# Optimization experiments

Measured on AMD Instinct MI355X. Metric: run time of the kernel, lower is better.

Reference implementation:

```python
import jax, jax.numpy as jnp
import numpy as np

N_NODES = 50000
N_EDGES = 150000
EMB = 64
IN_DIM = 32
LN_EPS = 1e-5


def setup_inputs() -> dict:
    key = jax.random.key(0)
    k1, k2, k3, k4 = jax.random.split(key, 4)
    h = jax.random.normal(k1, (N_NODES, EMB), dtype=jnp.float32)
    edge_attr = jax.random.normal(k2, (N_EDGES, IN_DIM), dtype=jnp.float32)
    edge_index = jax.random.randint(k3, (2, N_EDGES), 0, N_NODES, dtype=jnp.int64)
    # xavier_uniform for [EMB*EMB, IN_DIM] weight
    limit = float(np.sqrt(6.0 / (EMB * EMB + IN_DIM)))
    W = jax.random.uniform(k4, (EMB * EMB, IN_DIM), dtype=jnp.float32,
                           minval=-limit, maxval=limit)
    b = jnp.zeros((EMB * EMB,), dtype=jnp.float32)
    gamma = jnp.ones((EMB,), dtype=jnp.float32)
    beta = jnp.zeros((EMB,), dtype=jnp.float32)
    return {"h": h, "edge_attr": edge_attr, "W": W, "b": b,
            "gamma": gamma, "beta": beta, "edge_index": edge_index}


def reference(h, edge_attr, W, b, gamma, beta, edge_index):
    M = edge_attr.shape[0]
    E = h.shape[1]
    # per-edge transform matrix from edge features: [M, E, E]
    m = (edge_attr @ W.T + b).reshape(M, E, E)
    # gather target-node features and apply per-edge matvec: [M, E]
    h_j = h[edge_index[1]]
    msg = jnp.einsum('mef,mf->me', m, h_j)
    # scatter-add messages to source nodes
    aggr = jax.ops.segment_sum(msg, edge_index[0], num_segments=h.shape[0])
    # residual + LayerNorm
    x = h + aggr
    mu = jnp.mean(x, axis=-1, keepdims=True)
    var = jnp.mean(jnp.square(x - mu), axis=-1, keepdims=True)
    y = (x - mu) * jax.lax.rsqrt(var + LN_EPS)
    return y * gamma + beta
```

## Files before the change

kernel.cpp:

```cpp
#include <hip/hip_runtime.h>
#include <math.h>

#define N_NODES 50000
#define N_EDGES 150000
#define LN_EPS 1e-5f

#define BM 256
#define WM 64

typedef _Float16 f16x8 __attribute__((ext_vector_type(8)));
typedef _Float16 f16x4 __attribute__((ext_vector_type(4)));
typedef _Float16 f16x2 __attribute__((ext_vector_type(2)));
typedef float    f32x4 __attribute__((ext_vector_type(4)));

static __device__ __forceinline__ f16x2 pkrtz(float a, float b) {
    auto p = __builtin_amdgcn_cvt_pkrtz(a, b);
    f16x2 r; r[0] = (_Float16)p[0]; r[1] = (_Float16)p[1];
    return r;
}

__global__ void setup_kernel(const float* __restrict__ W, const float* __restrict__ b,
                             const float* __restrict__ h,
                             f16x8* __restrict__ WtF, float* __restrict__ out) {
    int bid = blockIdx.x;
    if (bid < 66) {
        int tid = bid * 256 + threadIdx.x;
        int l  = tid & 63;
        int nb = (tid >> 6) & 3;
        int c  = tid >> 8;
        int k0 = (l >> 4) << 3;
        int e  = nb * 16 + (l & 15);
        const float* src = (c < 64) ? &W[(e * 64 + c) * 32 + k0]
                                    : &b[e * 64 + (c - 64) * 32 + k0];
        float4 v0 = *(const float4*)src;
        float4 v1 = *(const float4*)(src + 4);
        f16x8 o;
        o[0] = (_Float16)v0.x; o[1] = (_Float16)v0.y; o[2] = (_Float16)v0.z; o[3] = (_Float16)v0.w;
        o[4] = (_Float16)v1.x; o[5] = (_Float16)v1.y; o[6] = (_Float16)v1.z; o[7] = (_Float16)v1.w;
        WtF[tid] = o;
    } else {
        int tid = (bid - 66) * 256 + threadIdx.x;
        ((float4*)out)[tid] = ((const float4*)h)[tid];
    }
}

__launch_bounds__(512, 4)
__global__ void edge_kernel(const float* __restrict__ ea,
                            const float* __restrict__ h,
                            const int*   __restrict__ ei,
                            const f16x8* __restrict__ WtF,
                            float* __restrict__ out)
{
    __shared__ _Float16 s_hj[BM][68];
    __shared__ int      s_src[BM];

    const int t = threadIdx.x;
    const int m_base = blockIdx.x * BM;

    {
        int row  = t >> 1;
        int half = t & 1;
        int gm   = m_base + row;
        if (gm < N_EDGES) {
            if (half == 0) s_src[row] = ei[gm];
            const float4* hr = (const float4*)&h[(size_t)ei[N_EDGES + gm] * 64 + half * 32];
            #pragma unroll
            for (int j = 0; j < 8; ++j) {
                float4 v = hr[j];
                f16x2 p0 = pkrtz(v.x, v.y);
                f16x2 p1 = pkrtz(v.z, v.w);
                f16x4 o; o[0] = p0[0]; o[1] = p0[1]; o[2] = p1[0]; o[3] = p1[1];
                *(f16x4*)&s_hj[row][half * 32 + j * 4] = o;
            }
        } else {
            if (half == 0) s_src[row] = -1;
            f16x4 z = (f16x4){0, 0, 0, 0};
            #pragma unroll
            for (int j = 0; j < 8; ++j)
                *(f16x4*)&s_hj[row][half * 32 + j * 4] = z;
        }
    }

    const int lane = t & 63;
    const int wid  = t >> 6;
    const int wrow = wid & 3;
    const int wn   = wid >> 2;
    const int nb0  = wn * 2;
    const int r16  = lane & 15;
    const int g    = lane >> 4;
    const int k0   = g * 8;
    const int row0 = wrow * WM;
    int rows[4];
    #pragma unroll
    for (int a = 0; a < 4; ++a) rows[a] = row0 + a * 16 + r16;

    f16x2 eap[4][4];
    #pragma unroll
    for (int a = 0; a < 4; ++a) {
        int gm = m_base + rows[a];
        if (gm < N_EDGES) {
            float4 v0 = *(const float4*)&ea[(size_t)gm * 32 + k0];
            float4 v1 = *(const float4*)&ea[(size_t)gm * 32 + k0 + 4];
            eap[a][0] = pkrtz(v0.x, v0.y);
            eap[a][1] = pkrtz(v0.z, v0.w);
            eap[a][2] = pkrtz(v1.x, v1.y);
            eap[a][3] = pkrtz(v1.z, v1.w);
        } else {
            #pragma unroll
            for (int i = 0; i < 4; ++i) eap[a][i] = (f16x2){0, 0};
        }
    }

    f32x4 acc[4][2];
    #pragma unroll
    for (int a = 0; a < 4; ++a)
        #pragma unroll
        for (int nb = 0; nb < 2; ++nb)
            acc[a][nb] = (f32x4){0.f, 0.f, 0.f, 0.f};

    __syncthreads();

    f16x8 b0[2], b1[2], b2[2];
    #pragma unroll
    for (int j = 0; j < 2; ++j) b0[j] = WtF[(0 * 4 + nb0 + j) * 64 + lane];
    #pragma unroll
    for (int j = 0; j < 2; ++j) b1[j] = WtF[(1 * 4 + nb0 + j) * 64 + lane];
    #pragma unroll
    for (int j = 0; j < 2; ++j) b2[j] = WtF[(2 * 4 + nb0 + j) * 64 + lane];

    _Float16 hc[4];
    #pragma unroll
    for (int a = 0; a < 4; ++a) hc[a] = s_hj[rows[a]][0];

    auto step = [&](int c, f16x8* bb, bool loadnext) {
        _Float16 hn[4] = {0, 0, 0, 0};
        if (loadnext) {
            #pragma unroll
            for (int a = 0; a < 4; ++a) hn[a] = s_hj[rows[a]][c + 1];
        }
        #pragma unroll
        for (int a = 0; a < 4; ++a) {
            f16x2 hs; hs[0] = hc[a]; hs[1] = hc[a];
            f16x2 p0 = eap[a][0] * hs;
            f16x2 p1 = eap[a][1] * hs;
            f16x2 p2 = eap[a][2] * hs;
            f16x2 p3 = eap[a][3] * hs;
            f16x8 va;
            va[0] = p0[0]; va[1] = p0[1]; va[2] = p1[0]; va[3] = p1[1];
            va[4] = p2[0]; va[5] = p2[1]; va[6] = p3[0]; va[7] = p3[1];
            #pragma unroll
            for (int j = 0; j < 2; ++j)
                acc[a][j] = __builtin_amdgcn_mfma_f32_16x16x32_f16(va, bb[j], acc[a][j], 0, 0, 0);
        }
        #pragma unroll
        for (int a = 0; a < 4; ++a) hc[a] = hn[a];
    };

    for (int c = 0; c < 63; c += 3) {
        step(c, b0, true);
        #pragma unroll
        for (int j = 0; j < 2; ++j) b0[j] = WtF[((c + 3) * 4 + nb0 + j) * 64 + lane];
        step(c + 1, b1, true);
        #pragma unroll
        for (int j = 0; j < 2; ++j) b1[j] = WtF[((c + 4) * 4 + nb0 + j) * 64 + lane];
        step(c + 2, b2, true);
        #pragma unroll
        for (int j = 0; j < 2; ++j) b2[j] = WtF[((c + 5) * 4 + nb0 + j) * 64 + lane];
    }
    step(63, b0, false);

    #pragma unroll
    for (int half = 0; half < 2; ++half) {
        f16x8* bb = half ? b2 : b1;
        #pragma unroll
        for (int a = 0; a < 4; ++a) {
            f16x4 lo = *(const f16x4*)&s_hj[rows[a]][half * 32 + k0];
            f16x4 hi = *(const f16x4*)&s_hj[rows[a]][half * 32 + k0 + 4];
            f16x8 va;
            va[0] = lo[0]; va[1] = lo[1]; va[2] = lo[2]; va[3] = lo[3];
            va[4] = hi[0]; va[5] = hi[1]; va[6] = hi[2]; va[7] = hi[3];
            #pragma unroll
            for (int j = 0; j < 2; ++j)
                acc[a][j] = __builtin_amdgcn_mfma_f32_16x16x32_f16(va, bb[j], acc[a][j], 0, 0, 0);
        }
    }

    #pragma unroll
    for (int a = 0; a < 4; ++a) {
        #pragma unroll
        for (int r = 0; r < 4; ++r) {
            int srcn = s_src[row0 + a * 16 + g * 4 + r];
            if (srcn >= 0) {
                #pragma unroll
                for (int j = 0; j < 2; ++j)
                    atomicAdd(&out[(size_t)srcn * 64 + (nb0 + j) * 16 + r16], acc[a][j][r]);
            }
        }
    }
}

__global__ void ln_kernel(const float* __restrict__ gamma, const float* __restrict__ beta,
                          float* __restrict__ out) {
    int row = blockIdx.x * 4 + (threadIdx.x >> 6);
    int lane = threadIdx.x & 63;
    if (row >= N_NODES) return;
    float x = out[row * 64 + lane];
    float s = x;
    #pragma unroll
    for (int o = 32; o; o >>= 1) s += __shfl_xor(s, o);
    float mu = s * (1.0f / 64.0f);
    float d = x - mu;
    float v = d * d;
    #pragma unroll
    for (int o = 32; o; o >>= 1) v += __shfl_xor(v, o);
    float var = v * (1.0f / 64.0f);
    float r = rsqrtf(var + LN_EPS);
    out[row * 64 + lane] = d * r * gamma[lane] + beta[lane];
}

extern "C" void kernel_launch(void* const* d_in, const int* in_sizes, int n_in,
                              void* d_out, int out_size, void* d_ws, size_t ws_size,
                              hipStream_t stream) {
    const float* h     = (const float*)d_in[0];
    const float* ea    = (const float*)d_in[1];
    const float* W     = (const float*)d_in[2];
    const float* b     = (const float*)d_in[3];
    const float* gamma = (const float*)d_in[4];
    const float* beta  = (const float*)d_in[5];
    const int*   ei    = (const int*)d_in[6];
    float* out = (float*)d_out;

    f16x8* WtF = (f16x8*)d_ws;

    setup_kernel<<<66 + 3125, 256, 0, stream>>>(W, b, h, WtF, out);
    edge_kernel<<<(N_EDGES + BM - 1) / BM, 512, 0, stream>>>(ea, h, ei, WtF, out);
    ln_kernel<<<(N_NODES + 3) / 4, 256, 0, stream>>>(gamma, beta, out);
}
```

Before: 163.0 us.

## Stage weights in LDS with double buffering, re-split warps, vectorize LayerNorm

The edge kernel now gives each warp 32 rows across all 64 output columns. It cooperatively stages the fp16 weight tiles into shared memory with double buffering and a block barrier per group of four columns, where before each warp read its own weight fragments straight from global memory. The bias tile is staged once into LDS. LayerNorm now uses 16 lanes per row with float4 accesses, and the copy of h processes two float4 per thread with bounds checks. This cuts redundant global/L2 weight traffic but adds LDS usage (about 68KB per block) and 16 barriers, which may lower occupancy.

Result: faster. 157.7 us (-3.2%).

```diff
diff --git a/kernel.cpp b/kernel.cpp
--- a/kernel.cpp
+++ b/kernel.cpp
@@ -6,7 +6,6 @@
 #define LN_EPS 1e-5f
 
 #define BM 256
-#define WM 64
 
 typedef _Float16 f16x8 __attribute__((ext_vector_type(8)));
 typedef _Float16 f16x4 __attribute__((ext_vector_type(4)));
@@ -39,8 +38,10 @@
         o[4] = (_Float16)v1.x; o[5] = (_Float16)v1.y; o[6] = (_Float16)v1.z; o[7] = (_Float16)v1.w;
         WtF[tid] = o;
     } else {
-        int tid = (bid - 66) * 256 + threadIdx.x;
-        ((float4*)out)[tid] = ((const float4*)h)[tid];
+        int base = (bid - 66) * 512 + threadIdx.x;
+        if (base < 800000) ((float4*)out)[base] = ((const float4*)h)[base];
+        int base2 = base + 256;
+        if (base2 < 800000) ((float4*)out)[base2] = ((const float4*)h)[base2];
     }
 }
 
@@ -53,6 +54,8 @@
 {
     __shared__ _Float16 s_hj[BM][68];
     __shared__ int      s_src[BM];
+    __shared__ f16x8    s_b[2][1024];
+    __shared__ f16x8    s_bias[512];
 
     const int t = threadIdx.x;
     const int m_base = blockIdx.x * BM;
@@ -83,20 +86,17 @@
 
     const int lane = t & 63;
     const int wid  = t >> 6;
-    const int wrow = wid & 3;
-    const int wn   = wid >> 2;
-    const int nb0  = wn * 2;
     const int r16  = lane & 15;
     const int g    = lane >> 4;
     const int k0   = g * 8;
-    const int row0 = wrow * WM;
-    int rows[4];
-    #pragma unroll
-    for (int a = 0; a < 4; ++a) rows[a] = row0 + a * 16 + r16;
-
-    f16x2 eap[4][4];
-    #pragma unroll
-    for (int a = 0; a < 4; ++a) {
+    const int row0 = wid * 32;
+    int rows[2];
+    rows[0] = row0 + r16;
+    rows[1] = row0 + 16 + r16;
+
+    f16x2 eap[2][4];
+    #pragma unroll
+    for (int a = 0; a < 2; ++a) {
         int gm = m_base + rows[a];
         if (gm < N_EDGES) {
             float4 v0 = *(const float4*)&ea[(size_t)gm * 32 + k0];
@@ -111,89 +111,90 @@
         }
     }
 
-    f32x4 acc[4][2];
-    #pragma unroll
-    for (int a = 0; a < 4; ++a)
-        #pragma unroll
-        for (int nb = 0; nb < 2; ++nb)
+    f32x4 acc[2][4];
+    #pragma unroll
+    for (int a = 0; a < 2; ++a)
+        #pragma unroll
+        for (int nb = 0; nb < 4; ++nb)
             acc[a][nb] = (f32x4){0.f, 0.f, 0.f, 0.f};
 
+    {
+        f16x8 rb = WtF[16384 + t];
+        f16x8 r0 = WtF[t];
+        f16x8 r1 = WtF[512 + t];
+        s_bias[t]        = rb;
+        s_b[0][t]        = r0;
+        s_b[0][512 + t]  = r1;
+    }
+
     __syncthreads();
 
-    f16x8 b0[2], b1[2], b2[2];
-    #pragma unroll
-    for (int j = 0; j < 2; ++j) b0[j] = WtF[(0 * 4 + nb0 + j) * 64 + lane];
-    #pragma unroll
-    for (int j = 0; j < 2; ++j) b1[j] = WtF[(1 * 4 + nb0 + j) * 64 + lane];
-    #pragma unroll
-    for (int j = 0; j < 2; ++j) b2[j] = WtF[(2 * 4 + nb0 + j) * 64 + lane];
-
-    _Float16 hc[4];
-    #pragma unroll
-    for (int a = 0; a < 4; ++a) hc[a] = s_hj[rows[a]][0];
-
-    auto step = [&](int c, f16x8* bb, bool loadnext) {
-        _Float16 hn[4] = {0, 0, 0, 0};
-        if (loadnext) {
-            #pragma unroll
-            for (int a = 0; a < 4; ++a) hn[a] = s_hj[rows[a]][c + 1];
-        }
-        #pragma unroll
-        for (int a = 0; a < 4; ++a) {
-            f16x2 hs; hs[0] = hc[a]; hs[1] = hc[a];
-            f16x2 p0 = eap[a][0] * hs;
-            f16x2 p1 = eap[a][1] * hs;
-            f16x2 p2 = eap[a][2] * hs;
-            f16x2 p3 = eap[a][3] * hs;
-            f16x8 va;
-            va[0] = p0[0]; va[1] = p0[1]; va[2] = p1[0]; va[3] = p1[1];
-            va[4] = p2[0]; va[5] = p2[1]; va[6] = p3[0]; va[7] = p3[1];
-            #pragma unroll
-            for (int j = 0; j < 2; ++j)
-                acc[a][j] = __builtin_amdgcn_mfma_f32_16x16x32_f16(va, bb[j], acc[a][j], 0, 0, 0);
-        }
-        #pragma unroll
-        for (int a = 0; a < 4; ++a) hc[a] = hn[a];
-    };
-
-    for (int c = 0; c < 63; c += 3) {
-        step(c, b0, true);
-        #pragma unroll
-        for (int j = 0; j < 2; ++j) b0[j] = WtF[((c + 3) * 4 + nb0 + j) * 64 + lane];
-        step(c + 1, b1, true);
-        #pragma unroll
-        for (int j = 0; j < 2; ++j) b1[j] = WtF[((c + 4) * 4 + nb0 + j) * 64 + lane];
-        step(c + 2, b2, true);
-        #pragma unroll
-        for (int j = 0; j < 2; ++j) b2[j] = WtF[((c + 5) * 4 + nb0 + j) * 64 + lane];
-    }
-    step(63, b0, false);
+    int buf = 0;
+    for (int grp = 0; grp < 16; ++grp) {
+        f16x8 ra, rb2;
+        if (grp < 15) {
+            ra  = WtF[(grp + 1) * 1024 + t];
+            rb2 = WtF[(grp + 1) * 1024 + 512 + t];
+        }
+        f16x4 hv[2];
+        hv[0] = *(const f16x4*)&s_hj[rows[0]][grp * 4];
+        hv[1] = *(const f16x4*)&s_hj[rows[1]][grp * 4];
+
+        #pragma unroll
+        for (int cc = 0; cc < 4; ++cc) {
+            f16x8 bf[4];
+            #pragma unroll
+            for (int nb = 0; nb < 4; ++nb)
+                bf[nb] = s_b[buf][(cc * 4 + nb) * 64 + lane];
+            #pragma unroll
+            for (int a = 0; a < 2; ++a) {
+                f16x2 hs; hs[0] = hv[a][cc]; hs[1] = hv[a][cc];
+                f16x2 p0 = eap[a][0] * hs;
+                f16x2 p1 = eap[a][1] * hs;
+                f16x2 p2 = eap[a][2] * hs;
+                f16x2 p3 = eap[a][3] * hs;
+                f16x8 va;
+                va[0] = p0[0]; va[1] = p0[1]; va[2] = p1[0]; va[3] = p1[1];
+                va[4] = p2[0]; va[5] = p2[1]; va[6] = p3[0]; va[7] = p3[1];
+                #pragma unroll
+                for (int nb = 0; nb < 4; ++nb)
+                    acc[a][nb] = __builtin_amdgcn_mfma_f32_16x16x32_f16(va, bf[nb], acc[a][nb], 0, 0, 0);
+            }
+        }
+        if (grp < 15) {
+            s_b[buf ^ 1][t]       = ra;
+            s_b[buf ^ 1][512 + t] = rb2;
+        }
+        __syncthreads();
+        buf ^= 1;
+    }
 
     #pragma unroll
     for (int half = 0; half < 2; ++half) {
-        f16x8* bb = half ? b2 : b1;
-        #pragma unroll
-        for (int a = 0; a < 4; ++a) {
+        #pragma unroll
+        for (int a = 0; a < 2; ++a) {
             f16x4 lo = *(const f16x4*)&s_hj[rows[a]][half * 32 + k0];
             f16x4 hi = *(const f16x4*)&s_hj[rows[a]][half * 32 + k0 + 4];
             f16x8 va;
             va[0] = lo[0]; va[1] = lo[1]; va[2] = lo[2]; va[3] = lo[3];
             va[4] = hi[0]; va[5] = hi[1]; va[6] = hi[2]; va[7] = hi[3];
             #pragma unroll
-            for (int j = 0; j < 2; ++j)
-                acc[a][j] = __builtin_amdgcn_mfma_f32_16x16x32_f16(va, bb[j], acc[a][j], 0, 0, 0);
-        }
-    }
-
-    #pragma unroll
-    for (int a = 0; a < 4; ++a) {
+            for (int nb = 0; nb < 4; ++nb) {
+                f16x8 bf = s_bias[(half * 4 + nb) * 64 + lane];
+                acc[a][nb] = __builtin_amdgcn_mfma_f32_16x16x32_f16(va, bf, acc[a][nb], 0, 0, 0);
+            }
+        }
+    }
+
+    #pragma unroll
+    for (int a = 0; a < 2; ++a) {
         #pragma unroll
         for (int r = 0; r < 4; ++r) {
             int srcn = s_src[row0 + a * 16 + g * 4 + r];
             if (srcn >= 0) {
                 #pragma unroll
-                for (int j = 0; j < 2; ++j)
-                    atomicAdd(&out[(size_t)srcn * 64 + (nb0 + j) * 16 + r16], acc[a][j][r]);
+                for (int nb = 0; nb < 4; ++nb)
+                    atomicAdd(&out[(size_t)srcn * 64 + nb * 16 + r16], acc[a][nb][r]);
             }
         }
     }
@@ -201,21 +202,27 @@
 
 __global__ void ln_kernel(const float* __restrict__ gamma, const float* __restrict__ beta,
                           float* __restrict__ out) {
-    int row = blockIdx.x * 4 + (threadIdx.x >> 6);
-    int lane = threadIdx.x & 63;
-    if (row >= N_NODES) return;
-    float x = out[row * 64 + lane];
-    float s = x;
-    #pragma unroll
-    for (int o = 32; o; o >>= 1) s += __shfl_xor(s, o);
-    float mu = s * (1.0f / 64.0f);
-    float d = x - mu;
-    float v = d * d;
-    #pragma unroll
-    for (int o = 32; o; o >>= 1) v += __shfl_xor(v, o);
-    float var = v * (1.0f / 64.0f);
-    float r = rsqrtf(var + LN_EPS);
-    out[row * 64 + lane] = d * r * gamma[lane] + beta[lane];
+    int t = threadIdx.x;
+    int row = blockIdx.x * 16 + (t >> 4);
+    int s = t & 15;
+    float4 v = *(float4*)&out[(size_t)row * 64 + s * 4];
+    float sum = v.x + v.y + v.z + v.w;
+    #pragma unroll
+    for (int o = 1; o < 16; o <<= 1) sum += __shfl_xor(sum, o);
+    float mu = sum * (1.0f / 64.0f);
+    float dx = v.x - mu, dy = v.y - mu, dz = v.z - mu, dw = v.w - mu;
+    float vs = dx * dx + dy * dy + dz * dz + dw * dw;
+    #pragma unroll
+    for (int o = 1; o < 16; o <<= 1) vs += __shfl_xor(vs, o);
+    float r = rsqrtf(vs * (1.0f / 64.0f) + LN_EPS);
+    float4 gv = *(const float4*)&gamma[s * 4];
+    float4 bv = *(const float4*)&beta[s * 4];
+    float4 o4;
+    o4.x = dx * r * gv.x + bv.x;
+    o4.y = dy * r * gv.y + bv.y;
+    o4.z = dz * r * gv.z + bv.z;
+    o4.w = dw * r * gv.w + bv.w;
+    *(float4*)&out[(size_t)row * 64 + s * 4] = o4;
 }
 
 extern "C" void kernel_launch(void* const* d_in, const int* in_sizes, int n_in,
@@ -232,7 +239,7 @@
 
     f16x8* WtF = (f16x8*)d_ws;
 
-    setup_kernel<<<66 + 3125, 256, 0, stream>>>(W, b, h, WtF, out);
+    setup_kernel<<<66 + 1563, 256, 0, stream>>>(W, b, h, WtF, out);
     edge_kernel<<<(N_EDGES + BM - 1) / BM, 512, 0, stream>>>(ea, h, ei, WtF, out);
-    ln_kernel<<<(N_NODES + 3) / 4, 256, 0, stream>>>(gamma, beta, out);
-}
+    ln_kernel<<<N_NODES / 16, 256, 0, stream>>>(gamma, beta, out);
+}
```
